# Performance work log

Measured on AMD Instinct MI355X. Metric: run time of the kernel, lower is better.

The kernel has to match this reference:

```python
import jax, jax.numpy as jnp
import numpy as np

XL, YL, XH, YH = 0.0, 0.0, 1000.0, 1000.0
NUM_MOVABLE = 1_000_000
NUM_FILLER = 200_000
NUM_NODES = NUM_MOVABLE + NUM_FILLER  # movable first, filler last (no fixed nodes)
RB_X = RB_Y = 512
PB_X = PB_Y = 512
MAX_ROUTE_RATE = 2.0
MIN_ROUTE_RATE = 1.0 / MAX_ROUTE_RATE
ROUTE_EXP = 2.5
MAX_PIN_RATE = 2.5
MIN_PIN_RATE = 1.0 / MAX_PIN_RATE
TOTAL_PLACE_AREA = 1.0e6
TOTAL_WHITESPACE = 5.0e5
AREA_STOP = 0.01
ROUTE_STOP = 0.01
PIN_STOP = 0.05
K = 3  # max bins a node can overlap per axis (node size < 2 * bin size)


def _bin_overlap_area(px, py, sx, sy, util, bsx, bsy, nbx, nby):
    """Per-node sum over overlapped bins of overlap_area * utilization.
    Faithful to adjust_node_area kernel: area_i = sum_b ovl_x * ovl_y * util[b]."""
    x_hi = px + sx
    y_hi = py + sy
    bx0 = jnp.floor((px - XL) / bsx).astype(jnp.int32)
    by0 = jnp.floor((py - YL) / bsy).astype(jnp.int32)
    ks = jnp.arange(K, dtype=jnp.int32)
    bx = bx0[:, None] + ks          # [N, K]
    by = by0[:, None] + ks
    bxc = jnp.clip(bx, 0, nbx - 1)
    byc = jnp.clip(by, 0, nby - 1)
    blx = XL + bxc.astype(util.dtype) * bsx
    bly = YL + byc.astype(util.dtype) * bsy
    ox = jnp.maximum(jnp.minimum(x_hi[:, None], blx + bsx) - jnp.maximum(px[:, None], blx), 0.0)
    oy = jnp.maximum(jnp.minimum(y_hi[:, None], bly + bsy) - jnp.maximum(py[:, None], bly), 0.0)
    ox = jnp.where((bx >= 0) & (bx < nbx), ox, 0.0)  # kill clipped duplicates
    oy = jnp.where((by >= 0) & (by < nby), oy, 0.0)
    u = util[bxc[:, :, None], byc[:, None, :]]       # [N, K, K] gather
    return jnp.einsum('nk,nl,nkl->n', ox, oy, u)


def setup_inputs() -> dict:
    key = jax.random.key(0)
    k1, k2, k3, k4, k5, k6, k7 = jax.random.split(key, 7)
    # sizes in [0.2, 1.2] (< bin size 1.953 -> each node spans <= 2 bins/axis)
    node_size_x = 0.2 + jax.random.uniform(k1, (NUM_NODES,), jnp.float32)
    node_size_y = 0.2 + jax.random.uniform(k2, (NUM_NODES,), jnp.float32)
    pos_x = jax.random.uniform(k3, (NUM_NODES,), jnp.float32) * (XH - 1.5)
    pos_y = jax.random.uniform(k4, (NUM_NODES,), jnp.float32) * (YH - 1.5)
    pos = jnp.concatenate([pos_x, pos_y])
    route_utilization_map = 0.5 + 1.3 * jax.random.uniform(k5, (RB_X, RB_Y), jnp.float32)
    pin_utilization_map = 0.3 + 1.7 * jax.random.uniform(k6, (PB_X, PB_Y), jnp.float32)
    pin_offset_x = jax.random.normal(k7, (1024,), jnp.float32)
    pin_offset_y = jax.random.normal(jax.random.fold_in(k7, 1), (1024,), jnp.float32)
    target_density = jnp.ones((1,), jnp.float32)
    return {
        'pos': pos,
        'node_size_x': node_size_x,
        'node_size_y': node_size_y,
        'pin_offset_x': pin_offset_x,
        'pin_offset_y': pin_offset_y,
        'target_density': target_density,
        'route_utilization_map': route_utilization_map,
        'pin_utilization_map': pin_utilization_map,
    }


def reference(pos, node_size_x, node_size_y, pin_offset_x, pin_offset_y,
              target_density, route_utilization_map, pin_utilization_map):
    num_nodes = NUM_NODES
    bsx_r = (XH - XL) / RB_X
    bsy_r = (YH - YL) / RB_Y
    bsx_p = (XH - XL) / PB_X
    bsy_p = (YH - YL) / PB_Y

    nsx_m = node_size_x[:NUM_MOVABLE]
    nsy_m = node_size_y[:NUM_MOVABLE]
    px_m = pos[:NUM_MOVABLE]
    py_m = pos[num_nodes:num_nodes + NUM_MOVABLE]
    old_area = nsx_m * nsy_m
    old_sum = old_area.sum()

    nsx_f = node_size_x[-NUM_FILLER:]
    nsy_f = node_size_y[-NUM_FILLER:]
    px_f = pos[num_nodes - NUM_FILLER:num_nodes]
    py_f = pos[2 * num_nodes - NUM_FILLER:]
    old_filler_sum = (nsx_f * nsy_f).sum()

    route_clamped = jnp.clip(route_utilization_map ** ROUTE_EXP, MIN_ROUTE_RATE, MAX_ROUTE_RATE)
    route_opt_area = _bin_overlap_area(px_m, py_m, nsx_m, nsy_m, route_clamped, bsx_r, bsy_r, RB_X, RB_Y)
    pin_clamped = jnp.clip(pin_utilization_map, MIN_PIN_RATE, MAX_PIN_RATE)
    pin_opt_area = _bin_overlap_area(px_m, py_m, nsx_m, nsy_m, pin_clamped, bsx_p, bsy_p, PB_X, PB_Y)

    area_increment = jax.nn.relu(jnp.maximum(route_opt_area, pin_opt_area) - old_area)
    inc_sum = area_increment.sum()
    budget = jnp.minimum(0.1 * TOTAL_WHITESPACE, TOTAL_PLACE_AREA - old_sum)
    raw_scale = budget / inc_sum
    scale = jnp.clip(raw_scale, 0.0, 1.0)
    new_area = jnp.where(raw_scale <= 0.0, old_area, old_area + area_increment * scale)
    inc_sum_eff = jnp.where(raw_scale <= 0.0, 0.0, inc_sum * scale)
    new_sum = old_sum + inc_sum_eff
    area_ratio = inc_sum_eff / old_sum

    route_flag = (jax.nn.relu(route_opt_area - old_area).sum() / old_sum) > ROUTE_STOP
    pin_flag = (jax.nn.relu(pin_opt_area - old_area).sum() / old_sum) > PIN_STOP
    adjust = (area_ratio > AREA_STOP) & (route_flag | pin_flag)

    # movable inflation, keeping node centers fixed
    mratio = jnp.sqrt(new_area / old_area)
    new_nsx_m = jnp.where(adjust, nsx_m * mratio, nsx_m)
    new_nsy_m = jnp.where(adjust, nsy_m * mratio, nsy_m)
    new_px_m = jnp.where(adjust, px_m + 0.5 * (nsx_m - new_nsx_m), px_m)
    new_py_m = jnp.where(adjust, py_m + 0.5 * (nsy_m - new_nsy_m), py_m)

    # filler shrink if total area overflows
    fcond = adjust & ((new_sum + old_filler_sum) > TOTAL_PLACE_AREA)
    fratio = jnp.sqrt(jax.nn.relu(TOTAL_PLACE_AREA - new_sum) / old_filler_sum)
    new_nsx_f = jnp.where(fcond, nsx_f * fratio, nsx_f)
    new_nsy_f = jnp.where(fcond, nsy_f * fratio, nsy_f)
    new_px_f = jnp.where(fcond, px_f + 0.5 * (nsx_f - new_nsx_f), px_f)
    new_py_f = jnp.where(fcond, py_f + 0.5 * (nsy_f - new_nsy_f), py_f)

    new_pos = jnp.concatenate([new_px_m, new_px_f, new_py_m, new_py_f])
    new_nsx = jnp.concatenate([new_nsx_m, new_nsx_f])
    new_nsy = jnp.concatenate([new_nsy_m, new_nsy_f])
    return (new_pos, new_nsx, new_nsy)
```

## Files before the change

### kernel.cpp

```cpp
#include <hip/hip_runtime.h>
#include <math.h>

#define NUM_MOVABLE 1000000
#define NUM_FILLER  200000
#define NUM_NODES   1200000
#define NBX 512
#define NBY 512
#define THREADS 256
#define NGROUPS 300000
#define MGROUPS 250000
#define P1_BLOCKS ((NGROUPS + THREADS - 1) / THREADS)

static constexpr float BSX = 1000.0f / 512.0f;
static constexpr float TOTAL_PLACE_AREA = 1000000.0f;
static constexpr float TOTAL_WHITESPACE = 500000.0f;
static constexpr float AREA_STOP  = 0.01f;
static constexpr float ROUTE_STOP = 0.01f;
static constexpr float PIN_STOP   = 0.05f;

__device__ __forceinline__ float route_val(float x) {
    return fminf(fmaxf(powf(x, 2.5f), 0.5f), 2.0f);
}
__device__ __forceinline__ float pin_val(float x) {
    return fminf(fmaxf(x, 0.4f), 2.5f);
}

__device__ __forceinline__ void block_reduce_store5(float v0, float v1, float v2,
                                                    float v3, float v4,
                                                    float4* d4, float* df) {
    __shared__ float red[4][5];
    #pragma unroll
    for (int o = 32; o >= 1; o >>= 1) {
        v0 += __shfl_down(v0, o, 64);
        v1 += __shfl_down(v1, o, 64);
        v2 += __shfl_down(v2, o, 64);
        v3 += __shfl_down(v3, o, 64);
        v4 += __shfl_down(v4, o, 64);
    }
    int wid = threadIdx.x >> 6, lid = threadIdx.x & 63;
    if (lid == 0) { red[wid][0] = v0; red[wid][1] = v1; red[wid][2] = v2;
                    red[wid][3] = v3; red[wid][4] = v4; }
    __syncthreads();
    if (threadIdx.x == 0) {
        float a0 = 0.f, a1 = 0.f, a2 = 0.f, a3 = 0.f, a4 = 0.f;
        for (int w = 0; w < 4; ++w) {
            a0 += red[w][0]; a1 += red[w][1]; a2 += red[w][2];
            a3 += red[w][3]; a4 += red[w][4];
        }
        *d4 = make_float4(a0, a1, a2, a3);
        *df = a4;
    }
}

__global__ void pass1_kernel(const float* __restrict__ pos,
                             const float* __restrict__ nsx,
                             const float* __restrict__ nsy,
                             const float* __restrict__ route,
                             const float* __restrict__ pin,
                             float* __restrict__ inc,
                             float4* __restrict__ part4,
                             float* __restrict__ partf) {
    int t = blockIdx.x * THREADS + threadIdx.x;
    float s_old = 0.f, s_inc = 0.f, s_r = 0.f, s_p = 0.f, sf = 0.f;

    if (t < MGROUPS) {
        float4 px4 = ((const float4*)pos)[t];
        float4 py4 = ((const float4*)(pos + NUM_NODES))[t];
        float4 sx4 = ((const float4*)nsx)[t];
        float4 sy4 = ((const float4*)nsy)[t];
        float ai4[4];
        #pragma unroll
        for (int j = 0; j < 4; ++j) {
            float px = (&px4.x)[j], py = (&py4.x)[j];
            float sx = (&sx4.x)[j], sy = (&sy4.x)[j];
            float hix = px + sx, hiy = py + sy;
            int b0x = (int)floorf(px / BSX);
            int b0y = (int)floorf(py / BSX);
            float ex = (float)(b0x + 1) * BSX;
            float ey = (float)(b0y + 1) * BSX;
            float wx0 = fminf(hix, ex) - px;
            float wx1 = fmaxf(hix - ex, 0.0f);
            float wy0 = fminf(hiy, ey) - py;
            float wy1 = fmaxf(hiy - ey, 0.0f);
            int bx1 = min(b0x + 1, NBX - 1);
            int by1 = min(b0y + 1, NBY - 1);
            int r0 = b0x * NBY, r1 = bx1 * NBY;

            float r00 = route_val(route[r0 + b0y]);
            float r01 = route_val(route[r0 + by1]);
            float r10 = route_val(route[r1 + b0y]);
            float r11 = route_val(route[r1 + by1]);
            float p00 = pin_val(pin[r0 + b0y]);
            float p01 = pin_val(pin[r0 + by1]);
            float p10 = pin_val(pin[r1 + b0y]);
            float p11 = pin_val(pin[r1 + by1]);

            float r = wx0 * (wy0 * r00 + wy1 * r01) + wx1 * (wy0 * r10 + wy1 * r11);
            float p = wx0 * (wy0 * p00 + wy1 * p01) + wx1 * (wy0 * p10 + wy1 * p11);

            float old_a = sx * sy;
            float ai = fmaxf(fmaxf(r, p) - old_a, 0.0f);
            ai4[j] = ai;
            s_old += old_a;
            s_inc += ai;
            s_r += fmaxf(r - old_a, 0.0f);
            s_p += fmaxf(p - old_a, 0.0f);
        }
        ((float4*)inc)[t] = make_float4(ai4[0], ai4[1], ai4[2], ai4[3]);
    } else if (t < NGROUPS) {
        float4 sx4 = ((const float4*)nsx)[t];
        float4 sy4 = ((const float4*)nsy)[t];
        sf = sx4.x * sy4.x + sx4.y * sy4.y + sx4.z * sy4.z + sx4.w * sy4.w;
    }
    block_reduce_store5(s_old, s_inc, s_r, s_p, sf,
                        part4 + blockIdx.x, partf + blockIdx.x);
}

__global__ void apply_kernel(const float* __restrict__ pos,
                             const float* __restrict__ nsx,
                             const float* __restrict__ nsy,
                             const float* __restrict__ inc,
                             const float4* __restrict__ part4,
                             const float* __restrict__ partf,
                             float* __restrict__ out) {
    __shared__ float red[4][5];
    __shared__ float der[4];
    {
        float t0 = 0.f, t1 = 0.f, t2 = 0.f, t3 = 0.f, t4 = 0.f;
        for (int b = threadIdx.x; b < P1_BLOCKS; b += THREADS) {
            float4 v = part4[b];
            t0 += v.x; t1 += v.y; t2 += v.z; t3 += v.w;
            t4 += partf[b];
        }
        #pragma unroll
        for (int o = 32; o >= 1; o >>= 1) {
            t0 += __shfl_down(t0, o, 64);
            t1 += __shfl_down(t1, o, 64);
            t2 += __shfl_down(t2, o, 64);
            t3 += __shfl_down(t3, o, 64);
            t4 += __shfl_down(t4, o, 64);
        }
        int wid = threadIdx.x >> 6, lid = threadIdx.x & 63;
        if (lid == 0) { red[wid][0] = t0; red[wid][1] = t1; red[wid][2] = t2;
                        red[wid][3] = t3; red[wid][4] = t4; }
        __syncthreads();
        if (threadIdx.x == 0) {
            float old_sum = 0.f, inc_sum = 0.f, route_ex = 0.f, pin_ex = 0.f, filler_sum = 0.f;
            for (int w = 0; w < 4; ++w) {
                old_sum += red[w][0]; inc_sum += red[w][1]; route_ex += red[w][2];
                pin_ex += red[w][3]; filler_sum += red[w][4];
            }
            float budget = fminf(0.1f * TOTAL_WHITESPACE, TOTAL_PLACE_AREA - old_sum);
            float raw = budget / inc_sum;
            float scale = fminf(fmaxf(raw, 0.0f), 1.0f);
            float scale_eff = (raw <= 0.0f) ? 0.0f : scale;
            float inc_eff = (raw <= 0.0f) ? 0.0f : inc_sum * scale;
            float new_sum = old_sum + inc_eff;
            float area_ratio = inc_eff / old_sum;
            bool route_flag = (route_ex / old_sum) > ROUTE_STOP;
            bool pin_flag = (pin_ex / old_sum) > PIN_STOP;
            bool adjust = (area_ratio > AREA_STOP) && (route_flag || pin_flag);
            bool fcond = adjust && (new_sum + filler_sum > TOTAL_PLACE_AREA);
            float fratio = sqrtf(fmaxf(TOTAL_PLACE_AREA - new_sum, 0.0f) / filler_sum);
            der[0] = adjust ? 1.0f : 0.0f;
            der[1] = scale_eff;
            der[2] = fcond ? 1.0f : 0.0f;
            der[3] = fratio;
        }
        __syncthreads();
    }
    const float adjust = der[0], scale_eff = der[1];
    const float fcond = der[2], fratio = der[3];

    int t = blockIdx.x * THREADS + threadIdx.x;
    if (t >= NGROUPS) return;

    float4 px4 = ((const float4*)pos)[t];
    float4 py4 = ((const float4*)(pos + NUM_NODES))[t];
    float4 sx4 = ((const float4*)nsx)[t];
    float4 sy4 = ((const float4*)nsy)[t];
    float nx[4], ny[4], opx[4], opy[4];

    if (t < MGROUPS) {
        float4 ai4 = ((const float4*)inc)[t];
        #pragma unroll
        for (int j = 0; j < 4; ++j) {
            float px = (&px4.x)[j], py = (&py4.x)[j];
            float sx = (&sx4.x)[j], sy = (&sy4.x)[j];
            nx[j] = sx; ny[j] = sy; opx[j] = px; opy[j] = py;
            if (adjust > 0.5f) {
                float old_a = sx * sy;
                float na = old_a + (&ai4.x)[j] * scale_eff;
                float mr = sqrtf(na / old_a);
                nx[j] = sx * mr; ny[j] = sy * mr;
                opx[j] = px + 0.5f * (sx - nx[j]);
                opy[j] = py + 0.5f * (sy - ny[j]);
            }
        }
    } else {
        #pragma unroll
        for (int j = 0; j < 4; ++j) {
            float px = (&px4.x)[j], py = (&py4.x)[j];
            float sx = (&sx4.x)[j], sy = (&sy4.x)[j];
            nx[j] = sx; ny[j] = sy; opx[j] = px; opy[j] = py;
            if (fcond > 0.5f) {
                nx[j] = sx * fratio; ny[j] = sy * fratio;
                opx[j] = px + 0.5f * (sx - nx[j]);
                opy[j] = py + 0.5f * (sy - ny[j]);
            }
        }
    }
    ((float4*)out)[t]                   = make_float4(opx[0], opx[1], opx[2], opx[3]);
    ((float4*)(out + NUM_NODES))[t]     = make_float4(opy[0], opy[1], opy[2], opy[3]);
    ((float4*)(out + 2 * NUM_NODES))[t] = make_float4(nx[0], nx[1], nx[2], nx[3]);
    ((float4*)(out + 3 * NUM_NODES))[t] = make_float4(ny[0], ny[1], ny[2], ny[3]);
}

extern "C" void kernel_launch(void* const* d_in, const int* in_sizes, int n_in,
                              void* d_out, int out_size, void* d_ws, size_t ws_size,
                              hipStream_t stream) {
    const float* pos       = (const float*)d_in[0];
    const float* node_sx   = (const float*)d_in[1];
    const float* node_sy   = (const float*)d_in[2];
    const float* route_map = (const float*)d_in[6];
    const float* pin_map   = (const float*)d_in[7];
    float* out = (float*)d_out;

    float*  ws    = (float*)d_ws;
    float*  inc   = ws;
    float4* part4 = (float4*)(inc + NUM_MOVABLE);
    float*  partf = (float*)(part4 + P1_BLOCKS);

    hipLaunchKernelGGL(pass1_kernel, dim3(P1_BLOCKS), dim3(THREADS), 0, stream,
                       pos, node_sx, node_sy, route_map, pin_map, inc, part4, partf);
    hipLaunchKernelGGL(apply_kernel, dim3(P1_BLOCKS), dim3(THREADS), 0, stream,
                       pos, node_sx, node_sy, inc, part4, partf, out);
}
```

Baseline: 126.3 us.

## Precompute fp16 2x2 bin-neighborhood quad map to replace per-node scattered gathers

```diff
diff --git a/kernel.cpp b/kernel.cpp
--- a/kernel.cpp
+++ b/kernel.cpp
@@ -1,4 +1,5 @@
 #include <hip/hip_runtime.h>
+#include <hip/hip_fp16.h>
 #include <math.h>
 
 #define NUM_MOVABLE 1000000
@@ -9,7 +10,9 @@
 #define THREADS 256
 #define NGROUPS 300000
 #define MGROUPS 250000
-#define P1_BLOCKS ((NGROUPS + THREADS - 1) / THREADS)
+#define PREP_BLOCKS 1024
+#define P1_BLOCKS ((MGROUPS + THREADS - 1) / THREADS)
+#define AP_BLOCKS ((NGROUPS + THREADS - 1) / THREADS)
 
 static constexpr float BSX = 1000.0f / 512.0f;
 static constexpr float TOTAL_PLACE_AREA = 1000000.0f;
@@ -18,57 +21,70 @@
 static constexpr float ROUTE_STOP = 0.01f;
 static constexpr float PIN_STOP   = 0.05f;
 
-__device__ __forceinline__ float route_val(float x) {
-    return fminf(fmaxf(powf(x, 2.5f), 0.5f), 2.0f);
-}
-__device__ __forceinline__ float pin_val(float x) {
-    return fminf(fmaxf(x, 0.4f), 2.5f);
-}
-
-__device__ __forceinline__ void block_reduce_store5(float v0, float v1, float v2,
-                                                    float v3, float v4,
-                                                    float4* d4, float* df) {
-    __shared__ float red[4][5];
+struct alignas(16) Quad { __half2 r0; __half2 r1; __half2 p0; __half2 p1; };
+
+__device__ __forceinline__ float route_val(const float* m, int idx) {
+    return fminf(fmaxf(powf(m[idx], 2.5f), 0.5f), 2.0f);
+}
+__device__ __forceinline__ float pin_val(const float* m, int idx) {
+    return fminf(fmaxf(m[idx], 0.4f), 2.5f);
+}
+
+__global__ void prep_kernel(const float* __restrict__ route,
+                            const float* __restrict__ pin,
+                            const float* __restrict__ nsx,
+                            const float* __restrict__ nsy,
+                            Quad* __restrict__ qmap,
+                            float* __restrict__ pf) {
+    int i = blockIdx.x * THREADS + threadIdx.x;
+    {
+        int bx = i >> 9, by = i & 511;
+        int bx1 = min(bx + 1, NBX - 1), by1 = min(by + 1, NBY - 1);
+        int i00 = bx * NBY + by,  i01 = bx * NBY + by1;
+        int i10 = bx1 * NBY + by, i11 = bx1 * NBY + by1;
+        Quad q;
+        q.r0 = __halves2half2(__float2half(route_val(route, i00)),
+                              __float2half(route_val(route, i01)));
+        q.r1 = __halves2half2(__float2half(route_val(route, i10)),
+                              __float2half(route_val(route, i11)));
+        q.p0 = __halves2half2(__float2half(pin_val(pin, i00)),
+                              __float2half(pin_val(pin, i01)));
+        q.p1 = __halves2half2(__float2half(pin_val(pin, i10)),
+                              __float2half(pin_val(pin, i11)));
+        qmap[i] = q;
+    }
+    float s = 0.f;
+    if (i < NUM_FILLER) {
+        int j = NUM_MOVABLE + i;
+        s = nsx[j] * nsy[j];
+    }
+    __shared__ float red[4];
     #pragma unroll
-    for (int o = 32; o >= 1; o >>= 1) {
-        v0 += __shfl_down(v0, o, 64);
-        v1 += __shfl_down(v1, o, 64);
-        v2 += __shfl_down(v2, o, 64);
-        v3 += __shfl_down(v3, o, 64);
-        v4 += __shfl_down(v4, o, 64);
-    }
+    for (int o = 32; o >= 1; o >>= 1) s += __shfl_down(s, o, 64);
     int wid = threadIdx.x >> 6, lid = threadIdx.x & 63;
-    if (lid == 0) { red[wid][0] = v0; red[wid][1] = v1; red[wid][2] = v2;
-                    red[wid][3] = v3; red[wid][4] = v4; }
+    if (lid == 0) red[wid] = s;
     __syncthreads();
-    if (threadIdx.x == 0) {
-        float a0 = 0.f, a1 = 0.f, a2 = 0.f, a3 = 0.f, a4 = 0.f;
-        for (int w = 0; w < 4; ++w) {
-            a0 += red[w][0]; a1 += red[w][1]; a2 += red[w][2];
-            a3 += red[w][3]; a4 += red[w][4];
-        }
-        *d4 = make_float4(a0, a1, a2, a3);
-        *df = a4;
-    }
+    if (threadIdx.x == 0)
+        pf[blockIdx.x] = red[0] + red[1] + red[2] + red[3];
 }
 
 __global__ void pass1_kernel(const float* __restrict__ pos,
                              const float* __restrict__ nsx,
                              const float* __restrict__ nsy,
-                             const float* __restrict__ route,
-                             const float* __restrict__ pin,
+                             const Quad* __restrict__ qmap,
                              float* __restrict__ inc,
-                             float4* __restrict__ part4,
-                             float* __restrict__ partf) {
+                             float4* __restrict__ part4) {
     int t = blockIdx.x * THREADS + threadIdx.x;
-    float s_old = 0.f, s_inc = 0.f, s_r = 0.f, s_p = 0.f, sf = 0.f;
+    float s_old = 0.f, s_inc = 0.f, s_r = 0.f, s_p = 0.f;
 
     if (t < MGROUPS) {
         float4 px4 = ((const float4*)pos)[t];
         float4 py4 = ((const float4*)(pos + NUM_NODES))[t];
         float4 sx4 = ((const float4*)nsx)[t];
         float4 sy4 = ((const float4*)nsy)[t];
-        float ai4[4];
+
+        Quad q[4];
+        float wx0[4], wx1[4], wy0[4], wy1[4];
         #pragma unroll
         for (int j = 0; j < 4; ++j) {
             float px = (&px4.x)[j], py = (&py4.x)[j];
@@ -78,26 +94,22 @@
             int b0y = (int)floorf(py / BSX);
             float ex = (float)(b0x + 1) * BSX;
             float ey = (float)(b0y + 1) * BSX;
-            float wx0 = fminf(hix, ex) - px;
-            float wx1 = fmaxf(hix - ex, 0.0f);
-            float wy0 = fminf(hiy, ey) - py;
-            float wy1 = fmaxf(hiy - ey, 0.0f);
-            int bx1 = min(b0x + 1, NBX - 1);
-            int by1 = min(b0y + 1, NBY - 1);
-            int r0 = b0x * NBY, r1 = bx1 * NBY;
-
-            float r00 = route_val(route[r0 + b0y]);
-            float r01 = route_val(route[r0 + by1]);
-            float r10 = route_val(route[r1 + b0y]);
-            float r11 = route_val(route[r1 + by1]);
-            float p00 = pin_val(pin[r0 + b0y]);
-            float p01 = pin_val(pin[r0 + by1]);
-            float p10 = pin_val(pin[r1 + b0y]);
-            float p11 = pin_val(pin[r1 + by1]);
-
-            float r = wx0 * (wy0 * r00 + wy1 * r01) + wx1 * (wy0 * r10 + wy1 * r11);
-            float p = wx0 * (wy0 * p00 + wy1 * p01) + wx1 * (wy0 * p10 + wy1 * p11);
-
+            wx0[j] = fminf(hix, ex) - px;
+            wx1[j] = fmaxf(hix - ex, 0.0f);
+            wy0[j] = fminf(hiy, ey) - py;
+            wy1[j] = fmaxf(hiy - ey, 0.0f);
+            q[j] = qmap[b0x * NBY + b0y];
+        }
+        float ai4[4];
+        #pragma unroll
+        for (int j = 0; j < 4; ++j) {
+            float2 r0 = __half22float2(q[j].r0), r1 = __half22float2(q[j].r1);
+            float2 p0 = __half22float2(q[j].p0), p1 = __half22float2(q[j].p1);
+            float r = wx0[j] * (wy0[j] * r0.x + wy1[j] * r0.y)
+                    + wx1[j] * (wy0[j] * r1.x + wy1[j] * r1.y);
+            float p = wx0[j] * (wy0[j] * p0.x + wy1[j] * p0.y)
+                    + wx1[j] * (wy0[j] * p1.x + wy1[j] * p1.y);
+            float sx = (&sx4.x)[j], sy = (&sy4.x)[j];
             float old_a = sx * sy;
             float ai = fmaxf(fmaxf(r, p) - old_a, 0.0f);
             ai4[j] = ai;
@@ -107,13 +119,27 @@
             s_p += fmaxf(p - old_a, 0.0f);
         }
         ((float4*)inc)[t] = make_float4(ai4[0], ai4[1], ai4[2], ai4[3]);
-    } else if (t < NGROUPS) {
-        float4 sx4 = ((const float4*)nsx)[t];
-        float4 sy4 = ((const float4*)nsy)[t];
-        sf = sx4.x * sy4.x + sx4.y * sy4.y + sx4.z * sy4.z + sx4.w * sy4.w;
-    }
-    block_reduce_store5(s_old, s_inc, s_r, s_p, sf,
-                        part4 + blockIdx.x, partf + blockIdx.x);
+    }
+
+    __shared__ float red[4][4];
+    #pragma unroll
+    for (int o = 32; o >= 1; o >>= 1) {
+        s_old += __shfl_down(s_old, o, 64);
+        s_inc += __shfl_down(s_inc, o, 64);
+        s_r   += __shfl_down(s_r, o, 64);
+        s_p   += __shfl_down(s_p, o, 64);
+    }
+    int wid = threadIdx.x >> 6, lid = threadIdx.x & 63;
+    if (lid == 0) { red[wid][0] = s_old; red[wid][1] = s_inc;
+                    red[wid][2] = s_r;   red[wid][3] = s_p; }
+    __syncthreads();
+    if (threadIdx.x == 0) {
+        float a0 = 0.f, a1 = 0.f, a2 = 0.f, a3 = 0.f;
+        for (int w = 0; w < 4; ++w) {
+            a0 += red[w][0]; a1 += red[w][1]; a2 += red[w][2]; a3 += red[w][3];
+        }
+        part4[blockIdx.x] = make_float4(a0, a1, a2, a3);
+    }
 }
 
 __global__ void apply_kernel(const float* __restrict__ pos,
@@ -121,7 +147,7 @@
                              const float* __restrict__ nsy,
                              const float* __restrict__ inc,
                              const float4* __restrict__ part4,
-                             const float* __restrict__ partf,
+                             const float* __restrict__ pf,
                              float* __restrict__ out) {
     __shared__ float red[4][5];
     __shared__ float der[4];
@@ -130,8 +156,8 @@
         for (int b = threadIdx.x; b < P1_BLOCKS; b += THREADS) {
             float4 v = part4[b];
             t0 += v.x; t1 += v.y; t2 += v.z; t3 += v.w;
-            t4 += partf[b];
-        }
+        }
+        for (int b = threadIdx.x; b < PREP_BLOCKS; b += THREADS) t4 += pf[b];
         #pragma unroll
         for (int o = 32; o >= 1; o >>= 1) {
             t0 += __shfl_down(t0, o, 64);
@@ -226,13 +252,16 @@
     const float* pin_map   = (const float*)d_in[7];
     float* out = (float*)d_out;
 
-    float*  ws    = (float*)d_ws;
-    float*  inc   = ws;
-    float4* part4 = (float4*)(inc + NUM_MOVABLE);
-    float*  partf = (float*)(part4 + P1_BLOCKS);
-
+    char*   ws    = (char*)d_ws;
+    Quad*   qmap  = (Quad*)ws;
+    float*  inc   = (float*)(ws + sizeof(Quad) * NBX * NBY);
+    float4* part4 = (float4*)((char*)inc + sizeof(float) * NUM_MOVABLE);
+    float*  pf    = (float*)(part4 + P1_BLOCKS);
+
+    hipLaunchKernelGGL(prep_kernel, dim3(PREP_BLOCKS), dim3(THREADS), 0, stream,
+                       route_map, pin_map, node_sx, node_sy, qmap, pf);
     hipLaunchKernelGGL(pass1_kernel, dim3(P1_BLOCKS), dim3(THREADS), 0, stream,
-                       pos, node_sx, node_sy, route_map, pin_map, inc, part4, partf);
-    hipLaunchKernelGGL(apply_kernel, dim3(P1_BLOCKS), dim3(THREADS), 0, stream,
-                       pos, node_sx, node_sy, inc, part4, partf, out);
-}
+                       pos, node_sx, node_sy, qmap, inc, part4);
+    hipLaunchKernelGGL(apply_kernel, dim3(AP_BLOCKS), dim3(THREADS), 0, stream,
+                       pos, node_sx, node_sy, inc, part4, pf, out);
+}
```

Measured after the change: 107.3 us. 1.18x faster.
